# Optimization experiments

Measured on AMD Instinct MI355X. Metric: run time of the kernel, lower is better.

## Reference

```python
import jax, jax.numpy as jnp
import numpy as np
from jax import lax

B, N = 4096, 512          # batch, sequence length (input_dim = 2*N)
H1, H2 = 64, 256          # hidden sizes of the two stacked LSTMs
E = 20                    # embed dim
OUT = 2


def _lstm_step(x, h, c, Wih, Whh, b):
    # gates in PyTorch order: i, f, g, o
    g = x @ Wih.T + h @ Whh.T + b
    i, f, gg, o = jnp.split(g, 4, axis=-1)
    c_new = jax.nn.sigmoid(f) * c + jax.nn.sigmoid(i) * jnp.tanh(gg)
    h_new = jax.nn.sigmoid(o) * jnp.tanh(c_new)
    return h_new, c_new


def setup_inputs() -> dict:
    key = jax.random.key(0)
    ks = jax.random.split(key, 9)
    s = lambda fan_in: 1.0 / np.sqrt(fan_in)
    return {
        "x": jax.random.normal(ks[0], (B, 2 * N), dtype=jnp.float32),
        "W_embed": jax.random.uniform(ks[1], (E, 2), minval=-s(2), maxval=s(2), dtype=jnp.float32),
        "Wih1": jax.random.uniform(ks[2], (4 * H1, E), minval=-s(H1), maxval=s(H1), dtype=jnp.float32),
        "Whh1": jax.random.uniform(ks[3], (4 * H1, H1), minval=-s(H1), maxval=s(H1), dtype=jnp.float32),
        "b1": jax.random.uniform(ks[4], (4 * H1,), minval=-s(H1), maxval=s(H1), dtype=jnp.float32),
        "Wih2": jax.random.uniform(ks[5], (4 * H2, H1), minval=-s(H2), maxval=s(H2), dtype=jnp.float32),
        "Whh2": jax.random.uniform(ks[6], (4 * H2, H2), minval=-s(H2), maxval=s(H2), dtype=jnp.float32),
        "b2": jax.random.uniform(ks[7], (4 * H2,), minval=-s(H2), maxval=s(H2), dtype=jnp.float32),
        "Wout": jax.random.uniform(ks[8], (OUT, H2), minval=-s(H2), maxval=s(H2), dtype=jnp.float32),
        "bout": jnp.zeros((OUT,), dtype=jnp.float32),
    }


def reference(x, W_embed, Wih1, Whh1, b1, Wih2, Whh2, b2, Wout, bout):
    b = x.shape[0]
    tokens = x.reshape(b, -1, 2).transpose(1, 0, 2)         # (n, b, 2)
    embedded = jax.nn.relu(tokens @ W_embed.T)              # (n, b, 20)

    def step(carry, xt):
        h, c = carry
        h, c = _lstm_step(xt, h, c, Wih1, Whh1, b1)
        return (h, c), None

    h0 = jnp.zeros((b, H1), dtype=x.dtype)
    (h64, _), _ = lax.scan(step, (h0, h0), embedded)        # last hidden (b, 64)

    # second LSTM applied to the 2-D last-hidden as a single timestep
    hz = jnp.zeros((b, H2), dtype=x.dtype)
    h256, _ = _lstm_step(h64, hz, hz, Wih2, Whh2, b2)       # (b, 256)

    return h256 @ Wout.T + bout                             # (b, 2)
```

## Files before the change

kernel.cpp:

```cpp
#include <hip/hip_runtime.h>

typedef _Float16 f16x8 __attribute__((ext_vector_type(8)));
typedef float    f32x4 __attribute__((ext_vector_type(4)));

#define NSTEP 512
#define LOG2E     1.4426950408889634f
#define TWOLOG2E  2.8853900817779268f

__device__ __forceinline__ float exp2_(float v) { return __builtin_amdgcn_exp2f(v); }

__device__ __forceinline__ float lstm_act_(float gi, float gf, float gg, float go, float& c) {
    float eg = exp2_(gg);
    float ei = exp2_(gi);
    float ef = exp2_(gf);
    float eo = exp2_(go);
    float X  = (eg + 1.0f) * (1.0f + ei);
    float Y  = 1.0f + ef;
    float r  = __builtin_amdgcn_rcpf(X * Y);
    c = fmaf(r * X, c, (eg - 1.0f) * (r * Y));
    float ec = exp2_(fminf(c * TWOLOG2E, 30.0f));
    float r2 = __builtin_amdgcn_rcpf((ec + 1.0f) * (1.0f + eo));
    return (ec - 1.0f) * r2;
}
__device__ __forceinline__ float sig_(float v) {
    return __builtin_amdgcn_rcpf(1.0f + exp2_(-v * LOG2E));
}
__device__ __forceinline__ float tanh_(float v) {
    return 1.0f - 2.0f * __builtin_amdgcn_rcpf(exp2_(v * TWOLOG2E) + 1.0f);
}

__global__ __launch_bounds__(1024, 1) void lstm_mfma16_kernel(
    const float* __restrict__ x,     const float* __restrict__ Wemb,
    const float* __restrict__ Wih1,  const float* __restrict__ Whh1,
    const float* __restrict__ b1,    const float* __restrict__ Wih2,
    const float* __restrict__ b2,    const float* __restrict__ Wout,
    const float* __restrict__ bout,  float* __restrict__ out)
{
    __shared__ __align__(16) _Float16 P[2][3][4][16][8];
    __shared__ __align__(16) float h2tmp[16 * 64];
    __shared__ __align__(16) float h2s[256 * 16];
    __shared__ float part[64 * 16 * 2];

    const int t   = threadIdx.x;
    const int l   = t & 63;
    const int tau = t >> 6;
    const int m   = l & 15;
    const int q   = l >> 4;
    const int b0  = blockIdx.x * 16;

    f16x8 wh[3];
    {
        const int g = m & 3;
        const float sc = (g == 2) ? TWOLOG2E : -LOG2E;
        const int n = g * 64 + 4 * tau + (m >> 2);
        #pragma unroll
        for (int c = 0; c < 3; ++c) {
            #pragma unroll
            for (int jj = 0; jj < 8; ++jj) {
                int k = c * 32 + (q << 3) + jj;
                float v = 0.0f;
                if (k < 20)      v = Wih1[n * 20 + k];
                else if (k < 84) v = Whh1[n * 64 + (k - 20)];
                wh[c][jj] = (_Float16)(v * sc);
            }
        }
    }
    f32x4 bias4;
    #pragma unroll
    for (int r = 0; r < 4; ++r) {
        float sc = (r == 2) ? TWOLOG2E : -LOG2E;
        bias4[r] = b1[r * 64 + 4 * tau + q] * sc;
    }
    const f32x4 z4 = {0.f, 0.f, 0.f, 0.f};

    const int myu = 4 * tau + q;
    const int wk  = 20 + myu;
    const int wkc = wk >> 5, wq = (wk >> 3) & 3, wjj = wk & 7;

    const bool embp = (l < 20);
    const int ee = l;
    const float* xrow = x + (size_t)(b0 + tau) * (2 * NSTEP);
    float we0 = 0.f, we1 = 0.f;
    if (embp) { we0 = Wemb[2 * l]; we1 = Wemb[2 * l + 1]; }

    for (int idx = t; idx < 2 * 3 * 4 * 16 * 8; idx += 1024)
        ((_Float16*)P)[idx] = (_Float16)0.0f;
    __syncthreads();
    if (embp)
        P[0][0][ee >> 3][tau][ee & 7] =
            (_Float16)fmaxf(xrow[0] * we0 + xrow[1] * we1, 0.0f);
    float xa = 0.f, xb = 0.f;
    if (embp) { xa = xrow[2]; xb = xrow[3]; }
    __syncthreads();

    float cst = 0.f;
    int cur = 0;

    for (int i = 0; i < NSTEP; ++i) {
        const _Float16* base = &P[cur][0][q][m][0];
        f16x8 f0 = *(const f16x8*)(base);
        f16x8 f1 = *(const f16x8*)(base + 512);
        f16x8 f2 = *(const f16x8*)(base + 1024);

        f32x4 a0 = __builtin_amdgcn_mfma_f32_16x16x32_f16(wh[0], f0, bias4, 0, 0, 0);
        f32x4 a1 = __builtin_amdgcn_mfma_f32_16x16x32_f16(wh[1], f1, z4, 0, 0, 0);
        a0 = __builtin_amdgcn_mfma_f32_16x16x32_f16(wh[2], f2, a0, 0, 0, 0);

        float hv = lstm_act_(a0[0] + a1[0], a0[1] + a1[1],
                             a0[2] + a1[2], a0[3] + a1[3], cst);

        const int nxt = cur ^ 1;
        P[nxt][wkc][wq][m][wjj] = (_Float16)hv;
        if (embp) {
            P[nxt][0][ee >> 3][tau][ee & 7] =
                (_Float16)fmaxf(fmaf(xa, we0, xb * we1), 0.0f);
            int ns = (i + 2 < NSTEP) ? i + 2 : NSTEP - 1;
            xa = xrow[2 * ns]; xb = xrow[2 * ns + 1];
        }
        __syncthreads();
        cur = nxt;
    }

    {
        int b = t >> 6, k = t & 63, kk = 20 + k;
        h2tmp[t] = (float)P[cur][kk >> 5][(kk >> 3) & 3][b][kk & 7];
    }
    __syncthreads();

    {
        const int u = t & 255;
        const int bh0 = (t >> 8) * 4;
        float acci[4], accg[4], acco[4];
        float bi2 = b2[u], bg2 = b2[512 + u], bo2 = b2[768 + u];
        #pragma unroll
        for (int b = 0; b < 4; ++b) { acci[b] = bi2; accg[b] = bg2; acco[b] = bo2; }
        for (int k4 = 0; k4 < 64; k4 += 4) {
            float4 wi = *(const float4*)&Wih2[(size_t)u * 64 + k4];
            float4 wg = *(const float4*)&Wih2[(size_t)(512 + u) * 64 + k4];
            float4 wo = *(const float4*)&Wih2[(size_t)(768 + u) * 64 + k4];
            #pragma unroll
            for (int b = 0; b < 4; ++b) {
                float4 hb = *(const float4*)&h2tmp[(bh0 + b) * 64 + k4];
                acci[b] += wi.x * hb.x + wi.y * hb.y + wi.z * hb.z + wi.w * hb.w;
                accg[b] += wg.x * hb.x + wg.y * hb.y + wg.z * hb.z + wg.w * hb.w;
                acco[b] += wo.x * hb.x + wo.y * hb.y + wo.z * hb.z + wo.w * hb.w;
            }
        }
        #pragma unroll
        for (int b = 0; b < 4; ++b) {
            float c2 = sig_(acci[b]) * tanh_(accg[b]);
            h2s[u * 16 + bh0 + b] = sig_(acco[b]) * tanh_(c2);
        }
    }
    __syncthreads();

    {
        int b = t & 15, grp = t >> 4;
        float p0 = 0.f, p1 = 0.f;
        #pragma unroll
        for (int uu = grp * 4; uu < grp * 4 + 4; ++uu) {
            float hvv = h2s[uu * 16 + b];
            p0 += hvv * Wout[uu];
            p1 += hvv * Wout[256 + uu];
        }
        part[(grp * 16 + b) * 2 + 0] = p0;
        part[(grp * 16 + b) * 2 + 1] = p1;
    }
    __syncthreads();
    if (t < 32) {
        int b = t >> 1, o = t & 1;
        float s0 = bout[o];
        for (int grp = 0; grp < 64; ++grp) s0 += part[(grp * 16 + b) * 2 + o];
        out[(size_t)(b0 + b) * 2 + o] = s0;
    }
}

extern "C" void kernel_launch(void* const* d_in, const int* in_sizes, int n_in,
                              void* d_out, int out_size, void* d_ws, size_t ws_size,
                              hipStream_t stream) {
    const float* x    = (const float*)d_in[0];
    const float* Wemb = (const float*)d_in[1];
    const float* Wih1 = (const float*)d_in[2];
    const float* Whh1 = (const float*)d_in[3];
    const float* b1   = (const float*)d_in[4];
    const float* Wih2 = (const float*)d_in[5];
    const float* b2   = (const float*)d_in[7];
    const float* Wout = (const float*)d_in[8];
    const float* bout = (const float*)d_in[9];
    float* out = (float*)d_out;

    lstm_mfma16_kernel<<<256, 1024, 0, stream>>>(
        x, Wemb, Wih1, Whh1, b1, Wih2, b2, Wout, bout, out);
}
```

Before: 317.2 us.

## Precompute input projections per 8-step chunk, shrinking the recurrent MFMA chain

The embedding and input-projection part of the LSTM gates is separated from the recurrence. For each chunk of 8 timesteps, the kernel computes embeddings for all steps at once into a shared buffer and runs the input MFMAs ahead of the serial loop. The recurrent step then only needs two dependent MFMAs over the 64-wide hidden state, using the precomputed input term as the accumulator. This is meant to shorten the per-step critical path and spread the global x loads across chunks, at the cost of more registers for the chunk accumulators and an extra barrier per chunk.

```diff
diff --git a/kernel.cpp b/kernel.cpp
--- a/kernel.cpp
+++ b/kernel.cpp
@@ -4,6 +4,8 @@
 typedef float    f32x4 __attribute__((ext_vector_type(4)));
 
 #define NSTEP 512
+#define CHUNK 8
+#define NCHUNK (NSTEP / CHUNK)
 #define LOG2E     1.4426950408889634f
 #define TWOLOG2E  2.8853900817779268f
 
@@ -36,7 +38,8 @@
     const float* __restrict__ b2,    const float* __restrict__ Wout,
     const float* __restrict__ bout,  float* __restrict__ out)
 {
-    __shared__ __align__(16) _Float16 P[2][3][4][16][8];
+    __shared__ __align__(16) _Float16 P[2][2][4][16][8];
+    __shared__ __align__(16) _Float16 Pe[CHUNK][4][16][8];
     __shared__ __align__(16) float h2tmp[16 * 64];
     __shared__ __align__(16) float h2s[256 * 16];
     __shared__ float part[64 * 16 * 2];
@@ -48,21 +51,21 @@
     const int q   = l >> 4;
     const int b0  = blockIdx.x * 16;
 
-    f16x8 wh[3];
+    f16x8 whh[2], whE;
     {
         const int g = m & 3;
         const float sc = (g == 2) ? TWOLOG2E : -LOG2E;
         const int n = g * 64 + 4 * tau + (m >> 2);
         #pragma unroll
-        for (int c = 0; c < 3; ++c) {
+        for (int c = 0; c < 2; ++c) {
             #pragma unroll
-            for (int jj = 0; jj < 8; ++jj) {
-                int k = c * 32 + (q << 3) + jj;
-                float v = 0.0f;
-                if (k < 20)      v = Wih1[n * 20 + k];
-                else if (k < 84) v = Whh1[n * 64 + (k - 20)];
-                wh[c][jj] = (_Float16)(v * sc);
-            }
+            for (int jj = 0; jj < 8; ++jj)
+                whh[c][jj] = (_Float16)(Whh1[n * 64 + c * 32 + (q << 3) + jj] * sc);
+        }
+        #pragma unroll
+        for (int jj = 0; jj < 8; ++jj) {
+            int k = (q << 3) + jj;
+            whE[jj] = (_Float16)((k < 20) ? Wih1[n * 20 + k] * sc : 0.0f);
         }
     }
     f32x4 bias4;
@@ -71,59 +74,71 @@
         float sc = (r == 2) ? TWOLOG2E : -LOG2E;
         bias4[r] = b1[r * 64 + 4 * tau + q] * sc;
     }
-    const f32x4 z4 = {0.f, 0.f, 0.f, 0.f};
 
     const int myu = 4 * tau + q;
-    const int wk  = 20 + myu;
-    const int wkc = wk >> 5, wq = (wk >> 3) & 3, wjj = wk & 7;
-
-    const bool embp = (l < 20);
-    const int ee = l;
-    const float* xrow = x + (size_t)(b0 + tau) * (2 * NSTEP);
-    float we0 = 0.f, we1 = 0.f;
-    if (embp) { we0 = Wemb[2 * l]; we1 = Wemb[2 * l + 1]; }
-
-    for (int idx = t; idx < 2 * 3 * 4 * 16 * 8; idx += 1024)
-        ((_Float16*)P)[idx] = (_Float16)0.0f;
-    __syncthreads();
-    if (embp)
-        P[0][0][ee >> 3][tau][ee & 7] =
-            (_Float16)fmaxf(xrow[0] * we0 + xrow[1] * we1, 0.0f);
-    float xa = 0.f, xb = 0.f;
-    if (embp) { xa = xrow[2]; xb = xrow[3]; }
-    __syncthreads();
-
-    float cst = 0.f;
-    int cur = 0;
-
-    for (int i = 0; i < NSTEP; ++i) {
-        const _Float16* base = &P[cur][0][q][m][0];
-        f16x8 f0 = *(const f16x8*)(base);
-        f16x8 f1 = *(const f16x8*)(base + 512);
-        f16x8 f2 = *(const f16x8*)(base + 1024);
-
-        f32x4 a0 = __builtin_amdgcn_mfma_f32_16x16x32_f16(wh[0], f0, bias4, 0, 0, 0);
-        f32x4 a1 = __builtin_amdgcn_mfma_f32_16x16x32_f16(wh[1], f1, z4, 0, 0, 0);
-        a0 = __builtin_amdgcn_mfma_f32_16x16x32_f16(wh[2], f2, a0, 0, 0, 0);
-
-        float hv = lstm_act_(a0[0] + a1[0], a0[1] + a1[1],
-                             a0[2] + a1[2], a0[3] + a1[3], cst);
-
-        const int nxt = cur ^ 1;
-        P[nxt][wkc][wq][m][wjj] = (_Float16)hv;
-        if (embp) {
-            P[nxt][0][ee >> 3][tau][ee & 7] =
-                (_Float16)fmaxf(fmaf(xa, we0, xb * we1), 0.0f);
-            int ns = (i + 2 < NSTEP) ? i + 2 : NSTEP - 1;
-            xa = xrow[2 * ns]; xb = xrow[2 * ns + 1];
+    _Float16* hw0 = &P[0][myu >> 5][(myu >> 3) & 3][m][myu & 7];
+
+    const float* xp[3]; _Float16* pe[3];
+    float we0[3], we1[3];
+    bool val[3];
+    float2 xv[3];
+    #pragma unroll
+    for (int k = 0; k < 3; ++k) {
+        int v  = t + 1024 * k;
+        val[k] = (v < CHUNK * 320);
+        int vv = val[k] ? v : 0;
+        int d  = vv % 20, pr = vv / 20;
+        int bb = pr & 15, s = pr >> 4;
+        we0[k] = Wemb[2 * d];
+        we1[k] = Wemb[2 * d + 1];
+        pe[k]  = &Pe[s][d >> 3][bb][d & 7];
+        xp[k]  = x + (size_t)(b0 + bb) * (2 * NSTEP) + 2 * s;
+        xv[k]  = *(const float2*)xp[k];
+    }
+
+    ((_Float16*)P)[t] = (_Float16)0.0f;
+    {
+        _Float16* pz = (_Float16*)Pe;
+        #pragma unroll
+        for (int k = 0; k < 4; ++k) pz[t + 1024 * k] = (_Float16)0.0f;
+    }
+    __syncthreads();
+
+    float cst = 0.0f;
+    for (int ch = 0; ch < NCHUNK; ++ch) {
+        #pragma unroll
+        for (int k = 0; k < 3; ++k)
+            if (val[k])
+                *pe[k] = (_Float16)fmaxf(fmaf(xv[k].x, we0[k], xv[k].y * we1[k]), 0.0f);
+        if (ch + 1 < NCHUNK) {
+            #pragma unroll
+            for (int k = 0; k < 3; ++k) { xp[k] += 16; xv[k] = *(const float2*)xp[k]; }
         }
         __syncthreads();
-        cur = nxt;
-    }
-
-    {
-        int b = t >> 6, k = t & 63, kk = 20 + k;
-        h2tmp[t] = (float)P[cur][kk >> 5][(kk >> 3) & 3][b][kk & 7];
+
+        f32x4 ax[CHUNK];
+        #pragma unroll
+        for (int j = 0; j < CHUNK; ++j) {
+            f16x8 fe = *(const f16x8*)&Pe[j][q][m][0];
+            ax[j] = __builtin_amdgcn_mfma_f32_16x16x32_f16(whE, fe, bias4, 0, 0, 0);
+        }
+
+        #pragma unroll
+        for (int j = 0; j < CHUNK; ++j) {
+            const int pr = j & 1;
+            f16x8 f0 = *(const f16x8*)&P[pr][0][q][m][0];
+            f16x8 f1 = *(const f16x8*)&P[pr][1][q][m][0];
+            f32x4 a = __builtin_amdgcn_mfma_f32_16x16x32_f16(whh[0], f0, ax[j], 0, 0, 0);
+            a = __builtin_amdgcn_mfma_f32_16x16x32_f16(whh[1], f1, a, 0, 0, 0);
+            float hv = lstm_act_(a[0], a[1], a[2], a[3], cst);
+            hw0[(pr ^ 1) * 1024] = (_Float16)hv;
+            __syncthreads();
+        }
+    }
+
+    {
+        int b = t >> 6, k = t & 63;
+        h2tmp[t] = (float)P[0][k >> 5][(k >> 3) & 3][b][k & 7];
     }
     __syncthreads();
 
```

New measurement: 310.0 us. 1.02x faster.
